# Performance work log

Measured on AMD Instinct MI355X. Metric: run time of the kernel, lower is better.

Reference implementation:

```python
import jax, jax.numpy as jnp
import numpy as np

B, T, CIN = 32, 16384, 32
COUT, NB, NA = 32, 3, 2


def setup_inputs() -> dict:
    key = jax.random.key(0)
    k1, k2, k3, k4 = jax.random.split(key, 4)
    u = jax.random.normal(k1, (B, T, CIN), dtype=jnp.float32)
    x0 = jax.random.normal(k2, (B, NA, COUT), dtype=jnp.float32)
    # AR coeffs scaled small so the length-16384 IIR recurrence is stable
    a_coeff = jax.random.normal(k3, (NA, COUT), dtype=jnp.float32) * 0.05
    b_coeff = jax.random.normal(k4, (NB, CIN, COUT), dtype=jnp.float32)
    return {"u": u, "x0": x0, "a_coeff": a_coeff, "b_coeff": b_coeff}


def reference(u, x0, a_coeff, b_coeff):
    # u: [B, T, CIN], x0: [B, NA, COUT]
    b, t, cin = u.shape
    n_a, cout = a_coeff.shape
    n_b = b_coeff.shape[0]
    a_f = jnp.flip(a_coeff, axis=0)   # [NA, COUT]
    b_f = jnp.flip(b_coeff, axis=0)   # [NB, CIN, COUT]

    def step(carry, ut):
        ubuf, xbuf = carry                                   # [NB,B,CIN], [NA,B,COUT]
        ubuf = jnp.concatenate([ubuf[1:], ut[None]], axis=0)  # push current input
        xt = jnp.einsum('to,tbo->bo', a_f, xbuf) + jnp.einsum('tio,tbi->bo', b_f, ubuf)
        xbuf = jnp.concatenate([xbuf[1:], xt[None]], axis=0)
        return (ubuf, xbuf), xt

    u0 = jnp.zeros((n_b, b, cin), dtype=u.dtype)
    x0_t = jnp.transpose(x0, (1, 0, 2))                      # [NA, B, COUT]
    _, ys = jax.lax.scan(step, (u0, x0_t), jnp.transpose(u, (1, 0, 2)), unroll=3)
    return jnp.transpose(ys, (1, 0, 2))                      # [B, T, COUT]
```

## Files before the change

### kernel.cpp

```cpp
#include <hip/hip_runtime.h>
#include <hip/hip_bf16.h>

namespace {

typedef short bf16x8 __attribute__((ext_vector_type(8), may_alias));
typedef unsigned long long u64_ma __attribute__((may_alias));
typedef __attribute__((ext_vector_type(16))) float f32x16;

constexpr int kB = 32, kT = 16384, kCin = 32, kCout = 32;
constexpr int kL = 128;
constexpr int kK = 32;
constexpr int kChunks = kT / kL;
constexpr int kWpB = 4;
constexpr int kRS = 80;
constexpr int kStageRows = 34;
constexpr int kStageB = kStageRows * kRS;

__device__ __forceinline__ unsigned bfbits(float f) {
  return (unsigned)__builtin_bit_cast(unsigned short, __float2bfloat16(f));
}

__global__ __launch_bounds__(256, 4) void mimo_mfma5(
    const float* __restrict__ u,
    const float* __restrict__ x0,
    const float* __restrict__ a_coeff,
    const float* __restrict__ b_coeff,
    float* __restrict__ out)
{
  __shared__ char lds[kWpB][kStageB];

  const int tidx = (int)threadIdx.x;
  const int lane = tidx & 63;
  const int col  = lane & 31;
  const int g    = lane >> 5;
  const int widx = tidx >> 6;
  const int wid  = (int)blockIdx.x * kWpB + widx;
  const int b     = wid >> 7;
  const int chunk = wid & (kChunks - 1);
  const int t0     = chunk * kL;
  const int tstart = chunk ? (t0 - kK) : 0;
  const int ntiles = (t0 + kL - tstart) >> 5;

  char* Lw = &lds[widx][0];

  bf16x8 Bf[3][2];
#pragma unroll
  for (int tau = 0; tau < 3; ++tau)
#pragma unroll
    for (int h = 0; h < 2; ++h) {
      const float* bp = b_coeff + (size_t)(2 - tau) * kCin * kCout
                        + (16 * g + 8 * h) * kCout + col;
      bf16x8 fr;
#pragma unroll
      for (int j = 0; j < 8; ++j)
        fr[j] = (short)__builtin_bit_cast(unsigned short, __float2bfloat16(bp[j * kCout]));
      Bf[tau][h] = fr;
    }

  const float a1 = a_coeff[col];
  const float a2 = a_coeff[kCout + col];
  float s1 = 0.f, s2 = 0.f;
  if (chunk == 0) {
    s1 = x0[(b * 2 + 1) * kCout + col];
    s2 = x0[(b * 2 + 0) * kCout + col];
  }

  const float* ub = u + (size_t)b * kT * kCin;
  float* ob = out + (size_t)b * kT * kCout;

  auto gload = [&](int rowbase, int f) -> float4 {
    const int grow = rowbase + (f >> 3);
    if (grow >= 0)
      return *(const float4*)(ub + (size_t)grow * kCin + ((f & 7) << 2));
    float4 z; z.x = 0.f; z.y = 0.f; z.z = 0.f; z.w = 0.f;
    return z;
  };
  auto stash = [&](int f, float4 v) {
    const unsigned lo = bfbits(v.x) | (bfbits(v.y) << 16);
    const unsigned hi = bfbits(v.z) | (bfbits(v.w) << 16);
    const unsigned long long q = ((unsigned long long)hi << 32) | lo;
    *(u64_ma*)(Lw + (f >> 3) * kRS + (f & 7) * 8) = q;
  };

  {
    const int rowbase = tstart - 2;
    float4 p0 = gload(rowbase, lane);
    float4 p1 = gload(rowbase, lane + 64);
    float4 p2 = gload(rowbase, lane + 128);
    float4 p3 = gload(rowbase, lane + 192);
    float4 p4;
    if (lane < 16) p4 = gload(rowbase, lane + 256);
    stash(lane, p0);
    stash(lane + 64, p1);
    stash(lane + 128, p2);
    stash(lane + 192, p3);
    if (lane < 16) stash(lane + 256, p4);
  }
  asm volatile("" ::: "memory");

  for (int tile = 0; tile < ntiles; ++tile) {
    const int tbase = tstart + 32 * tile;
    const bool last = (tile + 1 == ntiles);

    float4 n0, n1, n2, n3, n4;
    if (!last) {
      const int rowbase = tbase + 30;
      n0 = gload(rowbase, lane);
      n1 = gload(rowbase, lane + 64);
      n2 = gload(rowbase, lane + 128);
      n3 = gload(rowbase, lane + 192);
      if (lane < 16) n4 = gload(rowbase, lane + 256);
    }

    f32x16 acc;
#pragma unroll
    for (int i = 0; i < 16; ++i) acc[i] = 0.f;
#pragma unroll
    for (int tau = 0; tau < 3; ++tau) {
      const char* rp = Lw + (col + tau) * kRS + 32 * g;
#pragma unroll
      for (int h = 0; h < 2; ++h) {
        const bf16x8 fa = *(const bf16x8*)(rp + 16 * h);
        acc = __builtin_amdgcn_mfma_f32_32x32x16_bf16(fa, Bf[tau][h], acc, 0, 0, 0);
      }
    }

    float oth[16];
#pragma unroll
    for (int i = 0; i < 16; ++i) oth[i] = __shfl_xor(acc[i], 32);

    const bool owned = (tbase >= t0);
    float x1 = s1, x2 = s2;
#pragma unroll
    for (int j = 0; j < 32; ++j) {
      const int reg = 4 * (j >> 3) + (j & 3);
      const int g4  = (j >> 2) & 1;
      const float v = (g4 == g) ? acc[reg] : oth[reg];
      const float xn = fmaf(a1, x1, fmaf(a2, x2, v));
      if (owned && g4 == g) ob[(size_t)(tbase + j) * kCout + col] = xn;
      x2 = x1; x1 = xn;
    }
    s1 = x1; s2 = x2;

    if (!last) {
      asm volatile("" ::: "memory");
      stash(lane, n0);
      stash(lane + 64, n1);
      stash(lane + 128, n2);
      stash(lane + 192, n3);
      if (lane < 16) stash(lane + 256, n4);
      asm volatile("" ::: "memory");
    }
  }
}

}

extern "C" void kernel_launch(void* const* d_in, const int* in_sizes, int n_in,
                              void* d_out, int out_size, void* d_ws, size_t ws_size,
                              hipStream_t stream) {
  const float* u  = (const float*)d_in[0];
  const float* x0 = (const float*)d_in[1];
  const float* a  = (const float*)d_in[2];
  const float* bb = (const float*)d_in[3];
  float* out = (float*)d_out;

  dim3 grid(kB * kChunks / kWpB);
  dim3 block(256);
  hipLaunchKernelGGL(mimo_mfma5, grid, block, 0, stream, u, x0, a, bb, out);
}
```

Before: 29.80 us.

## Stage whole chunk input in LDS upfront instead of per-tile rolling buffer

```diff
diff --git a/kernel.cpp b/kernel.cpp
--- a/kernel.cpp
+++ b/kernel.cpp
@@ -13,14 +13,16 @@
 constexpr int kChunks = kT / kL;
 constexpr int kWpB = 4;
 constexpr int kRS = 80;
-constexpr int kStageRows = 34;
-constexpr int kStageB = kStageRows * kRS;
+constexpr int kRows = kK + kL + 2;
+constexpr int kStageB = kRows * kRS;
+constexpr int kF4 = kRows * 8;
+constexpr int kNT = 5;
 
 __device__ __forceinline__ unsigned bfbits(float f) {
   return (unsigned)__builtin_bit_cast(unsigned short, __float2bfloat16(f));
 }
 
-__global__ __launch_bounds__(256, 4) void mimo_mfma5(
+__global__ __launch_bounds__(256, 3) void mimo_mfma7(
     const float* __restrict__ u,
     const float* __restrict__ x0,
     const float* __restrict__ a_coeff,
@@ -38,8 +40,7 @@
   const int b     = wid >> 7;
   const int chunk = wid & (kChunks - 1);
   const int t0     = chunk * kL;
-  const int tstart = chunk ? (t0 - kK) : 0;
-  const int ntiles = (t0 + kL - tstart) >> 5;
+  const int tstart = t0 - kK;
 
   char* Lw = &lds[widx][0];
 
@@ -59,11 +60,12 @@
 
   const float a1 = a_coeff[col];
   const float a2 = a_coeff[kCout + col];
+  float i1 = 0.f, i2 = 0.f;
+  if (chunk == 0) {
+    i1 = x0[(b * 2 + 1) * kCout + col];
+    i2 = x0[(b * 2 + 0) * kCout + col];
+  }
   float s1 = 0.f, s2 = 0.f;
-  if (chunk == 0) {
-    s1 = x0[(b * 2 + 1) * kCout + col];
-    s2 = x0[(b * 2 + 0) * kCout + col];
-  }
 
   const float* ub = u + (size_t)b * kT * kCin;
   float* ob = out + (size_t)b * kT * kCout;
@@ -84,40 +86,27 @@
 
   {
     const int rowbase = tstart - 2;
-    float4 p0 = gload(rowbase, lane);
-    float4 p1 = gload(rowbase, lane + 64);
-    float4 p2 = gload(rowbase, lane + 128);
-    float4 p3 = gload(rowbase, lane + 192);
-    float4 p4;
-    if (lane < 16) p4 = gload(rowbase, lane + 256);
-    stash(lane, p0);
-    stash(lane + 64, p1);
-    stash(lane + 128, p2);
-    stash(lane + 192, p3);
-    if (lane < 16) stash(lane + 256, p4);
+#pragma unroll
+    for (int k = 0; k < kF4 / 64; ++k) {
+      const float4 p = gload(rowbase, lane + 64 * k);
+      stash(lane + 64 * k, p);
+    }
+    if (lane < (kF4 & 63)) {
+      const float4 p = gload(rowbase, lane + (kF4 & ~63));
+      stash(lane + (kF4 & ~63), p);
+    }
   }
   asm volatile("" ::: "memory");
 
-  for (int tile = 0; tile < ntiles; ++tile) {
+  for (int tile = 0; tile < kNT; ++tile) {
     const int tbase = tstart + 32 * tile;
-    const bool last = (tile + 1 == ntiles);
-
-    float4 n0, n1, n2, n3, n4;
-    if (!last) {
-      const int rowbase = tbase + 30;
-      n0 = gload(rowbase, lane);
-      n1 = gload(rowbase, lane + 64);
-      n2 = gload(rowbase, lane + 128);
-      n3 = gload(rowbase, lane + 192);
-      if (lane < 16) n4 = gload(rowbase, lane + 256);
-    }
 
     f32x16 acc;
 #pragma unroll
     for (int i = 0; i < 16; ++i) acc[i] = 0.f;
 #pragma unroll
     for (int tau = 0; tau < 3; ++tau) {
-      const char* rp = Lw + (col + tau) * kRS + 32 * g;
+      const char* rp = Lw + (32 * tile + col + tau) * kRS + 32 * g;
 #pragma unroll
       for (int h = 0; h < 2; ++h) {
         const bf16x8 fa = *(const bf16x8*)(rp + 16 * h);
@@ -128,6 +117,8 @@
     float oth[16];
 #pragma unroll
     for (int i = 0; i < 16; ++i) oth[i] = __shfl_xor(acc[i], 32);
+
+    if (chunk == 0 && tbase == t0) { s1 = i1; s2 = i2; }
 
     const bool owned = (tbase >= t0);
     float x1 = s1, x2 = s2;
@@ -141,16 +132,6 @@
       x2 = x1; x1 = xn;
     }
     s1 = x1; s2 = x2;
-
-    if (!last) {
-      asm volatile("" ::: "memory");
-      stash(lane, n0);
-      stash(lane + 64, n1);
-      stash(lane + 128, n2);
-      stash(lane + 192, n3);
-      if (lane < 16) stash(lane + 256, n4);
-      asm volatile("" ::: "memory");
-    }
   }
 }
 
@@ -167,5 +148,5 @@
 
   dim3 grid(kB * kChunks / kWpB);
   dim3 block(256);
-  hipLaunchKernelGGL(mimo_mfma5, grid, block, 0, stream, u, x0, a, bb, out);
+  hipLaunchKernelGGL(mimo_mfma7, grid, block, 0, stream, u, x0, a, bb, out);
 }
```

Result: slower. 35.43 us (+18.9%).

## Halve chunk length, share B fragments in LDS, and reuse halo rows

Applied to the files above, without the earlier changes.

```diff
diff --git a/kernel.cpp b/kernel.cpp
--- a/kernel.cpp
+++ b/kernel.cpp
@@ -8,26 +8,28 @@
 typedef __attribute__((ext_vector_type(16))) float f32x16;
 
 constexpr int kB = 32, kT = 16384, kCin = 32, kCout = 32;
-constexpr int kL = 128;
+constexpr int kL = 64;
 constexpr int kK = 32;
 constexpr int kChunks = kT / kL;
 constexpr int kWpB = 4;
 constexpr int kRS = 80;
 constexpr int kStageRows = 34;
 constexpr int kStageB = kStageRows * kRS;
+constexpr int kNT = 3;
 
 __device__ __forceinline__ unsigned bfbits(float f) {
   return (unsigned)__builtin_bit_cast(unsigned short, __float2bfloat16(f));
 }
 
-__global__ __launch_bounds__(256, 4) void mimo_mfma5(
+__global__ __launch_bounds__(256, 8) void mimo_mfma8(
     const float* __restrict__ u,
     const float* __restrict__ x0,
     const float* __restrict__ a_coeff,
     const float* __restrict__ b_coeff,
     float* __restrict__ out)
 {
-  __shared__ char lds[kWpB][kStageB];
+  __shared__ char stage[kWpB][kStageB];
+  __shared__ bf16x8 BfL[6][64];
 
   const int tidx = (int)threadIdx.x;
   const int lane = tidx & 63;
@@ -35,35 +37,38 @@
   const int g    = lane >> 5;
   const int widx = tidx >> 6;
   const int wid  = (int)blockIdx.x * kWpB + widx;
-  const int b     = wid >> 7;
+  const int b     = wid >> 8;
   const int chunk = wid & (kChunks - 1);
   const int t0     = chunk * kL;
-  const int tstart = chunk ? (t0 - kK) : 0;
-  const int ntiles = (t0 + kL - tstart) >> 5;
-
-  char* Lw = &lds[widx][0];
-
-  bf16x8 Bf[3][2];
-#pragma unroll
-  for (int tau = 0; tau < 3; ++tau)
-#pragma unroll
-    for (int h = 0; h < 2; ++h) {
-      const float* bp = b_coeff + (size_t)(2 - tau) * kCin * kCout
-                        + (16 * g + 8 * h) * kCout + col;
-      bf16x8 fr;
-#pragma unroll
-      for (int j = 0; j < 8; ++j)
-        fr[j] = (short)__builtin_bit_cast(unsigned short, __float2bfloat16(bp[j * kCout]));
-      Bf[tau][h] = fr;
-    }
+  const int tstart = t0 - kK;
+
+  char* Sw = &stage[widx][0];
+
+  if (widx == 0) {
+#pragma unroll
+    for (int tau = 0; tau < 3; ++tau)
+#pragma unroll
+      for (int h = 0; h < 2; ++h) {
+        const float* bp = b_coeff + (size_t)(2 - tau) * kCin * kCout
+                          + (16 * g + 8 * h) * kCout + col;
+        bf16x8 fr;
+#pragma unroll
+        for (int j = 0; j < 8; ++j)
+          fr[j] = (short)__builtin_bit_cast(unsigned short,
+                                            __float2bfloat16(bp[j * kCout]));
+        BfL[tau * 2 + h][lane] = fr;
+      }
+  }
+  __syncthreads();
 
   const float a1 = a_coeff[col];
   const float a2 = a_coeff[kCout + col];
+  float i1 = 0.f, i2 = 0.f;
+  if (chunk == 0) {
+    i1 = x0[(b * 2 + 1) * kCout + col];
+    i2 = x0[(b * 2 + 0) * kCout + col];
+  }
   float s1 = 0.f, s2 = 0.f;
-  if (chunk == 0) {
-    s1 = x0[(b * 2 + 1) * kCout + col];
-    s2 = x0[(b * 2 + 0) * kCout + col];
-  }
 
   const float* ub = u + (size_t)b * kT * kCin;
   float* ob = out + (size_t)b * kT * kCout;
@@ -79,7 +84,7 @@
     const unsigned lo = bfbits(v.x) | (bfbits(v.y) << 16);
     const unsigned hi = bfbits(v.z) | (bfbits(v.w) << 16);
     const unsigned long long q = ((unsigned long long)hi << 32) | lo;
-    *(u64_ma*)(Lw + (f >> 3) * kRS + (f & 7) * 8) = q;
+    *(u64_ma*)(Sw + (f >> 3) * kRS + (f & 7) * 8) = q;
   };
 
   {
@@ -98,18 +103,17 @@
   }
   asm volatile("" ::: "memory");
 
-  for (int tile = 0; tile < ntiles; ++tile) {
+  for (int tile = 0; tile < kNT; ++tile) {
     const int tbase = tstart + 32 * tile;
-    const bool last = (tile + 1 == ntiles);
-
-    float4 n0, n1, n2, n3, n4;
+    const bool last = (tile + 1 == kNT);
+
+    float4 n0, n1, n2, n3;
     if (!last) {
-      const int rowbase = tbase + 30;
+      const int rowbase = tbase + 32;
       n0 = gload(rowbase, lane);
       n1 = gload(rowbase, lane + 64);
       n2 = gload(rowbase, lane + 128);
       n3 = gload(rowbase, lane + 192);
-      if (lane < 16) n4 = gload(rowbase, lane + 256);
     }
 
     f32x16 acc;
@@ -117,38 +121,71 @@
     for (int i = 0; i < 16; ++i) acc[i] = 0.f;
 #pragma unroll
     for (int tau = 0; tau < 3; ++tau) {
-      const char* rp = Lw + (col + tau) * kRS + 32 * g;
+      const char* rp = Sw + (col + tau) * kRS + 32 * g;
 #pragma unroll
       for (int h = 0; h < 2; ++h) {
         const bf16x8 fa = *(const bf16x8*)(rp + 16 * h);
-        acc = __builtin_amdgcn_mfma_f32_32x32x16_bf16(fa, Bf[tau][h], acc, 0, 0, 0);
-      }
-    }
-
-    float oth[16];
-#pragma unroll
-    for (int i = 0; i < 16; ++i) oth[i] = __shfl_xor(acc[i], 32);
+        const bf16x8 fb = BfL[tau * 2 + h][lane];
+        acc = __builtin_amdgcn_mfma_f32_32x32x16_bf16(fa, fb, acc, 0, 0, 0);
+      }
+    }
+
+    if (chunk == 0 && tbase == t0) { s1 = i1; s2 = i2; }
 
     const bool owned = (tbase >= t0);
     float x1 = s1, x2 = s2;
 #pragma unroll
-    for (int j = 0; j < 32; ++j) {
-      const int reg = 4 * (j >> 3) + (j & 3);
-      const int g4  = (j >> 2) & 1;
-      const float v = (g4 == g) ? acc[reg] : oth[reg];
-      const float xn = fmaf(a1, x1, fmaf(a2, x2, v));
-      if (owned && g4 == g) ob[(size_t)(tbase + j) * kCout + col] = xn;
-      x2 = x1; x1 = xn;
+    for (int q = 0; q < 4; ++q) {
+      const float o0 = __shfl_xor(acc[4 * q + 0], 32);
+      const float o1 = __shfl_xor(acc[4 * q + 1], 32);
+      const float o2 = __shfl_xor(acc[4 * q + 2], 32);
+      const float o3 = __shfl_xor(acc[4 * q + 3], 32);
+      {
+        const float v0 = g ? o0 : acc[4 * q + 0];
+        const float v1 = g ? o1 : acc[4 * q + 1];
+        const float v2 = g ? o2 : acc[4 * q + 2];
+        const float v3 = g ? o3 : acc[4 * q + 3];
+        const float y0 = fmaf(a1, x1, fmaf(a2, x2, v0));
+        const float y1 = fmaf(a1, y0, fmaf(a2, x1, v1));
+        const float y2 = fmaf(a1, y1, fmaf(a2, y0, v2));
+        const float y3 = fmaf(a1, y2, fmaf(a2, y1, v3));
+        if (owned && g == 0) {
+          float* op = ob + (size_t)(tbase + 8 * q) * kCout + col;
+          op[0 * kCout] = y0; op[1 * kCout] = y1;
+          op[2 * kCout] = y2; op[3 * kCout] = y3;
+        }
+        x2 = y2; x1 = y3;
+      }
+      {
+        const float v0 = g ? acc[4 * q + 0] : o0;
+        const float v1 = g ? acc[4 * q + 1] : o1;
+        const float v2 = g ? acc[4 * q + 2] : o2;
+        const float v3 = g ? acc[4 * q + 3] : o3;
+        const float y0 = fmaf(a1, x1, fmaf(a2, x2, v0));
+        const float y1 = fmaf(a1, y0, fmaf(a2, x1, v1));
+        const float y2 = fmaf(a1, y1, fmaf(a2, y0, v2));
+        const float y3 = fmaf(a1, y2, fmaf(a2, y1, v3));
+        if (owned && g == 1) {
+          float* op = ob + (size_t)(tbase + 8 * q + 4) * kCout + col;
+          op[0 * kCout] = y0; op[1 * kCout] = y1;
+          op[2 * kCout] = y2; op[3 * kCout] = y3;
+        }
+        x2 = y2; x1 = y3;
+      }
     }
     s1 = x1; s2 = x2;
 
     if (!last) {
       asm volatile("" ::: "memory");
-      stash(lane, n0);
-      stash(lane + 64, n1);
-      stash(lane + 128, n2);
-      stash(lane + 192, n3);
-      if (lane < 16) stash(lane + 256, n4);
+      if (lane < 16) {
+        const int r = lane >> 3, cst = (lane & 7) * 8;
+        const u64_ma hv = *(const u64_ma*)(Sw + (32 + r) * kRS + cst);
+        *(u64_ma*)(Sw + r * kRS + cst) = hv;
+      }
+      stash(lane + 16, n0);
+      stash(lane + 16 + 64, n1);
+      stash(lane + 16 + 128, n2);
+      stash(lane + 16 + 192, n3);
       asm volatile("" ::: "memory");
     }
   }
@@ -167,5 +204,5 @@
 
   dim3 grid(kB * kChunks / kWpB);
   dim3 block(256);
-  hipLaunchKernelGGL(mimo_mfma5, grid, block, 0, stream, u, x0, a, bb, out);
-}
+  hipLaunchKernelGGL(mimo_mfma8, grid, block, 0, stream, u, x0, a, bb, out);
+}
```

After: 41.31 us. +38.6%, slower.

## Stage recurrence outputs in LDS for coalesced 16-byte stores and unroll tiles

Applied to the files above, without the earlier changes.

```diff
diff --git a/kernel.cpp b/kernel.cpp
--- a/kernel.cpp
+++ b/kernel.cpp
@@ -5,6 +5,7 @@
 
 typedef short bf16x8 __attribute__((ext_vector_type(8), may_alias));
 typedef unsigned long long u64_ma __attribute__((may_alias));
+typedef float f32x4_ma __attribute__((ext_vector_type(4), may_alias));
 typedef __attribute__((ext_vector_type(16))) float f32x16;
 
 constexpr int kB = 32, kT = 16384, kCin = 32, kCout = 32;
@@ -15,19 +16,23 @@
 constexpr int kRS = 80;
 constexpr int kStageRows = 34;
 constexpr int kStageB = kStageRows * kRS;
+constexpr int kNT = 5;
+constexpr int kTS = 36;
+constexpr int kTBufB = 32 * kTS * 4;
 
 __device__ __forceinline__ unsigned bfbits(float f) {
   return (unsigned)__builtin_bit_cast(unsigned short, __float2bfloat16(f));
 }
 
-__global__ __launch_bounds__(256, 4) void mimo_mfma5(
+__global__ __launch_bounds__(256, 4) void mimo_mfma10(
     const float* __restrict__ u,
     const float* __restrict__ x0,
     const float* __restrict__ a_coeff,
     const float* __restrict__ b_coeff,
     float* __restrict__ out)
 {
-  __shared__ char lds[kWpB][kStageB];
+  __shared__ char stage[kWpB][kStageB];
+  __shared__ char tbuf[kWpB][kTBufB];
 
   const int tidx = (int)threadIdx.x;
   const int lane = tidx & 63;
@@ -38,10 +43,10 @@
   const int b     = wid >> 7;
   const int chunk = wid & (kChunks - 1);
   const int t0     = chunk * kL;
-  const int tstart = chunk ? (t0 - kK) : 0;
-  const int ntiles = (t0 + kL - tstart) >> 5;
-
-  char* Lw = &lds[widx][0];
+  const int tstart = t0 - kK;
+
+  char* Sw = &stage[widx][0];
+  float* Tw = (float*)&tbuf[widx][0];
 
   bf16x8 Bf[3][2];
 #pragma unroll
@@ -59,11 +64,12 @@
 
   const float a1 = a_coeff[col];
   const float a2 = a_coeff[kCout + col];
+  float i1 = 0.f, i2 = 0.f;
+  if (chunk == 0) {
+    i1 = x0[(b * 2 + 1) * kCout + col];
+    i2 = x0[(b * 2 + 0) * kCout + col];
+  }
   float s1 = 0.f, s2 = 0.f;
-  if (chunk == 0) {
-    s1 = x0[(b * 2 + 1) * kCout + col];
-    s2 = x0[(b * 2 + 0) * kCout + col];
-  }
 
   const float* ub = u + (size_t)b * kT * kCin;
   float* ob = out + (size_t)b * kT * kCout;
@@ -79,7 +85,7 @@
     const unsigned lo = bfbits(v.x) | (bfbits(v.y) << 16);
     const unsigned hi = bfbits(v.z) | (bfbits(v.w) << 16);
     const unsigned long long q = ((unsigned long long)hi << 32) | lo;
-    *(u64_ma*)(Lw + (f >> 3) * kRS + (f & 7) * 8) = q;
+    *(u64_ma*)(Sw + (f >> 3) * kRS + (f & 7) * 8) = q;
   };
 
   {
@@ -98,9 +104,11 @@
   }
   asm volatile("" ::: "memory");
 
-  for (int tile = 0; tile < ntiles; ++tile) {
+#pragma unroll
+  for (int tile = 0; tile < kNT; ++tile) {
     const int tbase = tstart + 32 * tile;
-    const bool last = (tile + 1 == ntiles);
+    const bool last = (tile + 1 == kNT);
+    const bool owned = (tile >= 1);
 
     float4 n0, n1, n2, n3, n4;
     if (!last) {
@@ -117,7 +125,7 @@
     for (int i = 0; i < 16; ++i) acc[i] = 0.f;
 #pragma unroll
     for (int tau = 0; tau < 3; ++tau) {
-      const char* rp = Lw + (col + tau) * kRS + 32 * g;
+      const char* rp = Sw + (col + tau) * kRS + 32 * g;
 #pragma unroll
       for (int h = 0; h < 2; ++h) {
         const bf16x8 fa = *(const bf16x8*)(rp + 16 * h);
@@ -125,22 +133,52 @@
       }
     }
 
-    float oth[16];
-#pragma unroll
-    for (int i = 0; i < 16; ++i) oth[i] = __shfl_xor(acc[i], 32);
-
-    const bool owned = (tbase >= t0);
+    if (chunk == 0 && tile == 1) { s1 = i1; s2 = i2; }
+
     float x1 = s1, x2 = s2;
 #pragma unroll
-    for (int j = 0; j < 32; ++j) {
-      const int reg = 4 * (j >> 3) + (j & 3);
-      const int g4  = (j >> 2) & 1;
-      const float v = (g4 == g) ? acc[reg] : oth[reg];
-      const float xn = fmaf(a1, x1, fmaf(a2, x2, v));
-      if (owned && g4 == g) ob[(size_t)(tbase + j) * kCout + col] = xn;
-      x2 = x1; x1 = xn;
+    for (int q = 0; q < 4; ++q) {
+      const float o0 = __shfl_xor(acc[4 * q + 0], 32);
+      const float o1 = __shfl_xor(acc[4 * q + 1], 32);
+      const float o2 = __shfl_xor(acc[4 * q + 2], 32);
+      const float o3 = __shfl_xor(acc[4 * q + 3], 32);
+      const float va0 = g ? o0 : acc[4 * q + 0];
+      const float va1 = g ? o1 : acc[4 * q + 1];
+      const float va2 = g ? o2 : acc[4 * q + 2];
+      const float va3 = g ? o3 : acc[4 * q + 3];
+      const float ya0 = fmaf(a1, x1,  fmaf(a2, x2,  va0));
+      const float ya1 = fmaf(a1, ya0, fmaf(a2, x1,  va1));
+      const float ya2 = fmaf(a1, ya1, fmaf(a2, ya0, va2));
+      const float ya3 = fmaf(a1, ya2, fmaf(a2, ya1, va3));
+      const float vb0 = g ? acc[4 * q + 0] : o0;
+      const float vb1 = g ? acc[4 * q + 1] : o1;
+      const float vb2 = g ? acc[4 * q + 2] : o2;
+      const float vb3 = g ? acc[4 * q + 3] : o3;
+      const float yb0 = fmaf(a1, ya3, fmaf(a2, ya2, vb0));
+      const float yb1 = fmaf(a1, yb0, fmaf(a2, ya3, vb1));
+      const float yb2 = fmaf(a1, yb1, fmaf(a2, yb0, vb2));
+      const float yb3 = fmaf(a1, yb2, fmaf(a2, yb1, vb3));
+      x2 = yb2; x1 = yb3;
+      if (owned) {
+        const int rb = 8 * q + 4 * g;
+        Tw[(rb + 0) * kTS + col] = g ? yb0 : ya0;
+        Tw[(rb + 1) * kTS + col] = g ? yb1 : ya1;
+        Tw[(rb + 2) * kTS + col] = g ? yb2 : ya2;
+        Tw[(rb + 3) * kTS + col] = g ? yb3 : ya3;
+      }
     }
     s1 = x1; s2 = x2;
+
+    if (owned) {
+      asm volatile("" ::: "memory");
+#pragma unroll
+      for (int p = 0; p < 4; ++p) {
+        const f32x4_ma v = *(const f32x4_ma*)
+            ((const char*)Tw + (8 * p + (lane >> 3)) * (kTS * 4) + (lane & 7) * 16);
+        *(f32x4_ma*)(ob + (size_t)(tbase + 8 * p) * kCout + lane * 4) = v;
+      }
+      asm volatile("" ::: "memory");
+    }
 
     if (!last) {
       asm volatile("" ::: "memory");
@@ -167,5 +205,5 @@
 
   dim3 grid(kB * kChunks / kWpB);
   dim3 block(256);
-  hipLaunchKernelGGL(mimo_mfma5, grid, block, 0, stream, u, x0, a, bb, out);
-}
+  hipLaunchKernelGGL(mimo_mfma10, grid, block, 0, stream, u, x0, a, bb, out);
+}
```

Result: no change. 29.44 us (-1.2%).
